# Kernel optimization log

Measured on AMD Instinct MI355X. Metric: run time of the kernel, lower is better.

## Reference

```python
import jax, jax.numpy as jnp
import numpy as np
import math

EMBED_DIM = 1024
NUM_HEADS = 16
HEAD_DIM = EMBED_DIM // NUM_HEADS
B, S = 2, 2048


def setup_inputs() -> dict:
    key = jax.random.key(0)
    ks = jax.random.split(key, 13)
    sc = 1.0 / math.sqrt(EMBED_DIM)
    inp = {
        "query": jax.random.normal(ks[0], (B, S, EMBED_DIM), jnp.float32),
        "key": jax.random.normal(ks[1], (B, S, EMBED_DIM), jnp.float32),
        "value": jax.random.normal(ks[2], (B, S, EMBED_DIM), jnp.float32),
        "input_patch_mask": jax.random.randint(ks[3], (B, S), 0, 2, jnp.int32),
        "Wq": jax.random.normal(ks[4], (EMBED_DIM, EMBED_DIM), jnp.float32) * sc,
        "bq": jnp.zeros((EMBED_DIM,), jnp.float32),
        "Wk": jax.random.normal(ks[5], (EMBED_DIM, EMBED_DIM), jnp.float32) * sc,
        "bk": jnp.zeros((EMBED_DIM,), jnp.float32),
        "Wv": jax.random.normal(ks[6], (EMBED_DIM, EMBED_DIM), jnp.float32) * sc,
        "bv": jnp.zeros((EMBED_DIM,), jnp.float32),
        "Wo": jax.random.normal(ks[7], (EMBED_DIM, EMBED_DIM), jnp.float32) * sc,
        "bo": jnp.zeros((EMBED_DIM,), jnp.float32),
    }
    return inp


def _masked_softmax(scores, mask):
    # Equivalent to masked_fill(-inf) -> softmax -> nan_to_num(0.0):
    # fully-masked rows produce exactly 0, without generating NaNs.
    neg_inf = jnp.array(-jnp.inf, scores.dtype)
    s = jnp.where(mask, scores, neg_inf)
    m = jnp.max(s, axis=-1, keepdims=True)
    m_safe = jnp.where(jnp.isfinite(m), m, jnp.zeros_like(m))
    e = jnp.where(mask, jnp.exp(s - m_safe), 0.0)
    denom = jnp.sum(e, axis=-1, keepdims=True)
    denom = jnp.where(denom == 0.0, 1.0, denom)
    return e / denom


def reference(query, key, value, input_patch_mask, Wq, bq, Wk, bk, Wv, bv, Wo, bo):
    b, s, d = query.shape
    h, hd = NUM_HEADS, HEAD_DIM
    q = (query @ Wq.T + bq).reshape(b, s, h, hd).transpose(0, 2, 1, 3)  # [b,h,s,hd]
    k = (key @ Wk.T + bk).reshape(b, s, h, hd).transpose(0, 2, 1, 3)
    v = (value @ Wv.T + bv).reshape(b, s, h, hd).transpose(0, 2, 1, 3)
    scores = jnp.einsum("bhqd,bhkd->bhqk", q, k) / math.sqrt(hd)
    # mask[b,i,j] = patch_mask[b,i] * patch_mask[b,j]
    mask = (input_patch_mask[:, :, None] * input_patch_mask[:, None, :]) > 0
    attn = _masked_softmax(scores, mask[:, None, :, :])  # dropout in eval mode = identity
    context = jnp.einsum("bhqk,bhkd->bhqd", attn, v)
    context = context.transpose(0, 2, 1, 3).reshape(b, s, d)
    return context @ Wo.T + bo
```

## Files before the change

### kernel.cpp

```cpp
#include <hip/hip_runtime.h>
#include <cstdint>
#include <cstddef>

#define EMBED 1024
#define NHEAD 16
#define HD    64
#define BATCH 2
#define SEQ   2048
#define MROWS (BATCH*SEQ)
#define QSCALE 0.1803368801111137f

typedef __bf16 bf16;
typedef __bf16 bf16x8 __attribute__((ext_vector_type(8)));
typedef float  f32x4  __attribute__((ext_vector_type(4)));
typedef unsigned int u32;

#if __has_builtin(__builtin_amdgcn_exp2f)
#define EXP2(x) __builtin_amdgcn_exp2f(x)
#else
#define EXP2(x) exp2f(x)
#endif

typedef const u32 __attribute__((address_space(1)))* gp_t;
typedef u32 __attribute__((address_space(3)))* lp_t;

__device__ __forceinline__ void g2l16(const void* g, void* l) {
  __builtin_amdgcn_global_load_lds((gp_t)(uintptr_t)g, (lp_t)(u32)(uintptr_t)l, 16, 0, 0);
}

#define MFMA(a, b, c) __builtin_amdgcn_mfma_f32_16x16x32_bf16((a), (b), (c), 0, 0, 0)

#define SZX8 ((MROWS*EMBED)/8)
#define SZW8 ((EMBED*EMBED)/8)

__global__ void cast_all(const float* __restrict__ q, const float* __restrict__ k,
                         const float* __restrict__ v, const float* __restrict__ wq,
                         const float* __restrict__ wk, const float* __restrict__ wv,
                         const float* __restrict__ wo,
                         bf16* xq, bf16* xk, bf16* xv,
                         bf16* wqb, bf16* wkb, bf16* wvb, bf16* wob) {
  int z = blockIdx.y;
  const float* in; bf16* out;
  switch (z) {
    case 0: in = q;  out = xq;  break;
    case 1: in = k;  out = xk;  break;
    case 2: in = v;  out = xv;  break;
    case 3: in = wq; out = wqb; break;
    case 4: in = wk; out = wkb; break;
    case 5: in = wv; out = wvb; break;
    default: in = wo; out = wob; break;
  }
  int n8 = (z < 3) ? SZX8 : SZW8;
  int i = blockIdx.x * blockDim.x + threadIdx.x;
  if (i >= n8) return;
  const float4* p = (const float4*)in;
  float4 a = p[2*i], b = p[2*i+1];
  union { bf16 h[8]; uint4 u; } r;
  r.h[0] = (bf16)a.x; r.h[1] = (bf16)a.y; r.h[2] = (bf16)a.z; r.h[3] = (bf16)a.w;
  r.h[4] = (bf16)b.x; r.h[5] = (bf16)b.y; r.h[6] = (bf16)b.z; r.h[7] = (bf16)b.w;
  ((uint4*)out)[i] = r.u;
}

#define BM 128
#define BN 128
#define BK 32
#define NKI (EMBED/BK)

__device__ __forceinline__ void gemm_core(
    const bf16* __restrict__ A, const bf16* __restrict__ W,
    int m0, int n0, bf16* Al, bf16* Bl, f32x4 (&acc)[4][4])
{
  const int tid  = threadIdx.x;
  const int lane = tid & 63, wid = tid >> 6;
  const int quad = lane >> 4, l16 = lane & 15;
  const int wm = wid >> 1, wn = wid & 1;

  const int R = tid >> 2, Cc = tid & 3;
  const int gcol = (Cc ^ ((R >> 1) & 3)) * 8;
  const bf16* Ag = A + (size_t)(m0 + R) * EMBED + gcol;
  const bf16* Bg = W + (size_t)(n0 + R) * EMBED + gcol;
  bf16* AlW = Al + wid * 512;
  bf16* BlW = Bl + wid * 512;

  g2l16(Ag, AlW);                      g2l16(Ag + (size_t)64*EMBED, AlW + 2048);
  g2l16(Bg, BlW);                      g2l16(Bg + (size_t)64*EMBED, BlW + 2048);
  __syncthreads();

  for (int ki = 0; ki < NKI; ++ki) {
    const int cur = ki & 1;
    if (ki + 1 < NKI) {
      const int nb = cur ^ 1;
      const int k0 = (ki + 1) * BK;
      g2l16(Ag + k0, AlW + nb*4096);
      g2l16(Ag + (size_t)64*EMBED + k0, AlW + nb*4096 + 2048);
      g2l16(Bg + k0, BlW + nb*4096);
      g2l16(Bg + (size_t)64*EMBED + k0, BlW + nb*4096 + 2048);
    }
    const bf16* Ac = Al + cur*4096;
    const bf16* Bc = Bl + cur*4096;
    bf16x8 af[4], bg[4];
#pragma unroll
    for (int i = 0; i < 4; ++i) {
      int ra = wm*64 + i*16 + l16;
      af[i] = *(const bf16x8*)(Ac + ra*32 + ((quad ^ ((ra>>1)&3))*8));
      int rb = wn*64 + i*16 + l16;
      bg[i] = *(const bf16x8*)(Bc + rb*32 + ((quad ^ ((rb>>1)&3))*8));
    }
#pragma unroll
    for (int i = 0; i < 4; ++i)
#pragma unroll
      for (int j = 0; j < 4; ++j)
        acc[i][j] = MFMA(af[i], bg[j], acc[i][j]);
    __syncthreads();
  }
}

__global__ __launch_bounds__(256) void qkv_kernel(
    const bf16* __restrict__ Xq, const bf16* __restrict__ Xk, const bf16* __restrict__ Xv,
    const bf16* __restrict__ Wq, const bf16* __restrict__ Wk, const bf16* __restrict__ Wv,
    const float* __restrict__ bq, const float* __restrict__ bk, const float* __restrict__ bv,
    bf16* __restrict__ Qp, bf16* __restrict__ Kp, bf16* __restrict__ VTg)
{
  __shared__ bf16 Al[2*BM*BK];
  __shared__ bf16 Bl[2*BN*BK];
  const int z = blockIdx.z;
  const bf16* A = z==0 ? Xq : z==1 ? Xk : Wv;
  const bf16* W = z==0 ? Wq : z==1 ? Wk : Xv;
  const float* bias = z==0 ? bq : z==1 ? bk : bv;
  const float scale = (z==0) ? QSCALE : 1.0f;
  const int m0 = (z < 2) ? blockIdx.y * BM : blockIdx.x * BM;
  const int n0 = (z < 2) ? blockIdx.x * BN : blockIdx.y * BN;

  f32x4 acc[4][4] = {};
  gemm_core(A, W, m0, n0, Al, Bl, acc);

  const int lane = threadIdx.x & 63, wid = threadIdx.x >> 6;
  const int quad = lane >> 4, l16 = lane & 15;
  const int wm = wid >> 1, wn = wid & 1;

  if (z < 2) {
#pragma unroll
    for (int i = 0; i < 4; ++i) {
#pragma unroll
      for (int j = 0; j < 4; ++j) {
        int col = n0 + wn*64 + j*16 + l16;
        float bv2 = bias[col];
        bf16* outp = (z == 0) ? Qp : Kp;
#pragma unroll
        for (int r = 0; r < 4; ++r) {
          int row = m0 + wm*64 + i*16 + quad*4 + r;
          outp[(size_t)row*EMBED + col] = (bf16)((acc[i][j][r] + bv2) * scale);
        }
      }
    }
  } else {
    const int tcol0 = n0 + wn*64;
    const int bb   = tcol0 >> 11;
    const int tile = (tcol0 & (SEQ-1)) >> 6;
    const int rA = l16 & 3, qA = l16 >> 2;
    const int pbase = (rA>>1)*32 + qA*8 + (rA&1)*4;
#pragma unroll
    for (int i = 0; i < 4; ++i) {
      float4 bv4 = *(const float4*)&bias[m0 + wm*64 + i*16 + quad*4];
#pragma unroll
      for (int r = 0; r < 4; ++r) {
        int e = m0 + wm*64 + i*16 + quad*4 + r;
        int hh = e >> 6, dd = e & (HD-1);
        float bvr = (r==0) ? bv4.x : (r==1) ? bv4.y : (r==2) ? bv4.z : bv4.w;
        union { bf16 h[4]; uint2 uu; } pk;
#pragma unroll
        for (int j = 0; j < 4; ++j) pk.h[j] = (bf16)(acc[i][j][r] + bvr);
        *(uint2*)&VTg[(((size_t)bb*NHEAD + hh)*HD + dd)*SEQ + tile*64 + pbase] = pk.uu;
      }
    }
  }
}

__global__ __launch_bounds__(256) void oproj_kernel(
    const bf16* __restrict__ Ctx, const bf16* __restrict__ Wo,
    const float* __restrict__ bo, float* __restrict__ out)
{
  __shared__ bf16 Al[2*128*32];
  __shared__ bf16 Bl[2*64*32];
  const int tid  = threadIdx.x;
  const int lane = tid & 63, wid = tid >> 6;
  const int quad = lane >> 4, l16 = lane & 15;
  const int m0 = blockIdx.y * 128, n0 = blockIdx.x * 64;

  const int R = tid >> 2, Cc = tid & 3;
  const int gcol = (Cc ^ ((R >> 1) & 3)) * 8;
  const bf16* Ag = Ctx + (size_t)(m0 + R) * EMBED + gcol;
  const bf16* Bg = Wo  + (size_t)(n0 + R) * EMBED + gcol;
  bf16* AlW = Al + wid * 512;
  bf16* BlW = Bl + wid * 512;

  g2l16(Ag, AlW);  g2l16(Ag + (size_t)64*EMBED, AlW + 2048);
  g2l16(Bg, BlW);
  __syncthreads();

  f32x4 acc[2][4] = {};
  for (int ki = 0; ki < NKI; ++ki) {
    const int cur = ki & 1;
    if (ki + 1 < NKI) {
      const int nb = cur ^ 1;
      const int k0 = (ki + 1) * BK;
      g2l16(Ag + k0, AlW + nb*4096);
      g2l16(Ag + (size_t)64*EMBED + k0, AlW + nb*4096 + 2048);
      g2l16(Bg + k0, BlW + nb*2048);
    }
    const bf16* Ac = Al + cur*4096;
    const bf16* Bc = Bl + cur*2048;
    bf16x8 af[2], bg[4];
#pragma unroll
    for (int u = 0; u < 2; ++u) {
      int ra = wid*32 + u*16 + l16;
      af[u] = *(const bf16x8*)(Ac + ra*32 + ((quad ^ ((ra>>1)&3))*8));
    }
#pragma unroll
    for (int j = 0; j < 4; ++j) {
      int rb = j*16 + l16;
      bg[j] = *(const bf16x8*)(Bc + rb*32 + ((quad ^ ((rb>>1)&3))*8));
    }
#pragma unroll
    for (int u = 0; u < 2; ++u)
#pragma unroll
      for (int j = 0; j < 4; ++j)
        acc[u][j] = MFMA(af[u], bg[j], acc[u][j]);
    __syncthreads();
  }

#pragma unroll
  for (int u = 0; u < 2; ++u)
#pragma unroll
    for (int j = 0; j < 4; ++j) {
      int col = n0 + j*16 + l16;
      float bv = bo[col];
#pragma unroll
      for (int r = 0; r < 4; ++r) {
        int row = m0 + wid*32 + u*16 + quad*4 + r;
        out[(size_t)row*EMBED + col] = (acc[u][j][r] + bv);
      }
    }
}

#define NT  (SEQ/64)

__global__ __launch_bounds__(512, 2) void attn_kernel(
    const bf16* __restrict__ Qp, const bf16* __restrict__ Kp, const bf16* __restrict__ VT,
    const int* __restrict__ pmask, bf16* __restrict__ Ctx)
{
  __shared__ __align__(16) bf16 Kt[2][64*64];
  __shared__ __align__(16) bf16 Vt[3][64*64];

  const int qt = blockIdx.x, h = blockIdx.y, b = blockIdx.z;
  const int tid = threadIdx.x, lane = tid & 63, wid = tid >> 6;
  const int quad = lane >> 4, l16 = lane & 15;
  const int qrow0 = qt*128 + wid*16;

  const size_t qoff = (size_t)(b*SEQ + qrow0 + l16)*EMBED + h*HD;
  bf16x8 qf0 = *(const bf16x8*)(Qp + qoff + quad*8);
  bf16x8 qf1 = *(const bf16x8*)(Qp + qoff + 32 + quad*8);

  int qm[4];
#pragma unroll
  for (int r = 0; r < 4; ++r) qm[r] = pmask[b*SEQ + qrow0 + quad*4 + r];

  bf16 onev = (bf16)1.0f;
  bf16x8 ones = {onev, onev, onev, onev, onev, onev, onev, onev};

  const bf16* Kg  = Kp + (size_t)b*SEQ*EMBED + h*HD;
  const bf16* VTg = VT + (size_t)(b*NHEAD + h)*HD*SEQ;
  const int*  kmb = pmask + b*SEQ;

  const int R = tid >> 3;
  const int Cc = tid & 7;
  const int scol = (Cc ^ (R & 7)) * 8;

  f32x4 o[4] = {};
  f32x4 lacc = {};
  bf16x8 pa0 = {}, pa1 = {};

#define STAGE_K(kt, buf) g2l16(Kg + (size_t)((kt)*64 + R)*EMBED + scol, &Kt[buf][0] + wid*512)
#define STAGE_V(kt, buf) g2l16(VTg + (size_t)R*SEQ + (kt)*64 + scol,    &Vt[buf][0] + wid*512)

  STAGE_K(0, 0);
  STAGE_V(0, 0);
  __syncthreads();

  for (int kt = 0; kt < NT; ++kt) {
    if (kt + 1 < NT) {
      STAGE_K(kt + 1, (kt + 1) & 1);
      STAGE_V(kt + 1, (kt + 1) % 3);
    }

    const bf16* Kc = &Kt[kt & 1][0];
    f32x4 sg[4];
#pragma unroll
    for (int g = 0; g < 4; ++g) {
      int ra = g*16 + l16, sa = ra & 7;
      bf16x8 kfa = *(const bf16x8*)(Kc + ra*64 + ((quad     ^ sa)*8));
      bf16x8 kfb = *(const bf16x8*)(Kc + ra*64 + (((quad+4) ^ sa)*8));
      int4 kq = *(const int4*)(kmb + kt*64 + g*16 + quad*4);
      f32x4 s = {};
      s = MFMA(kfa, qf0, s);
      s = MFMA(kfb, qf1, s);
      sg[g][0] = kq.x ? EXP2(s[0]) : 0.0f;
      sg[g][1] = kq.y ? EXP2(s[1]) : 0.0f;
      sg[g][2] = kq.z ? EXP2(s[2]) : 0.0f;
      sg[g][3] = kq.w ? EXP2(s[3]) : 0.0f;
    }

    if (kt > 0) {
      const bf16* Vc = &Vt[(kt - 1) % 3][0];
      lacc = MFMA(pa0, ones, lacc);
      lacc = MFMA(pa1, ones, lacc);
#pragma unroll
      for (int t = 0; t < 4; ++t) {
        int rd = t*16 + l16, sd = rd & 7;
        bf16x8 vf0 = *(const bf16x8*)(Vc + rd*64 + ((quad     ^ sd)*8));
        bf16x8 vf1 = *(const bf16x8*)(Vc + rd*64 + (((quad+4) ^ sd)*8));
        o[t] = MFMA(pa0, vf0, o[t]);
        o[t] = MFMA(pa1, vf1, o[t]);
      }
    }

    pa0[0] = (bf16)sg[0][0]; pa0[1] = (bf16)sg[1][0]; pa0[2] = (bf16)sg[2][0]; pa0[3] = (bf16)sg[3][0];
    pa0[4] = (bf16)sg[0][1]; pa0[5] = (bf16)sg[1][1]; pa0[6] = (bf16)sg[2][1]; pa0[7] = (bf16)sg[3][1];
    pa1[0] = (bf16)sg[0][2]; pa1[1] = (bf16)sg[1][2]; pa1[2] = (bf16)sg[2][2]; pa1[3] = (bf16)sg[3][2];
    pa1[4] = (bf16)sg[0][3]; pa1[5] = (bf16)sg[1][3]; pa1[6] = (bf16)sg[2][3]; pa1[7] = (bf16)sg[3][3];

    __syncthreads();
  }

  {
    const bf16* Vc = &Vt[(NT - 1) % 3][0];
    lacc = MFMA(pa0, ones, lacc);
    lacc = MFMA(pa1, ones, lacc);
#pragma unroll
    for (int t = 0; t < 4; ++t) {
      int rd = t*16 + l16, sd = rd & 7;
      bf16x8 vf0 = *(const bf16x8*)(Vc + rd*64 + ((quad     ^ sd)*8));
      bf16x8 vf1 = *(const bf16x8*)(Vc + rd*64 + (((quad+4) ^ sd)*8));
      o[t] = MFMA(pa0, vf0, o[t]);
      o[t] = MFMA(pa1, vf1, o[t]);
    }
  }

  float inv[4];
#pragma unroll
  for (int r = 0; r < 4; ++r)
    inv[r] = (qm[r] && lacc[r] > 0.f) ? 1.0f / lacc[r] : 0.0f;

#pragma unroll
  for (int t = 0; t < 4; ++t)
#pragma unroll
    for (int r = 0; r < 4; ++r) {
      int row = b*SEQ + qrow0 + quad*4 + r;
      Ctx[(size_t)row*EMBED + h*HD + t*16 + l16] = (bf16)(o[t][r] * inv[r]);
    }
}

extern "C" void kernel_launch(void* const* d_in, const int* in_sizes, int n_in,
                              void* d_out, int out_size, void* d_ws, size_t ws_size,
                              hipStream_t stream)
{
  const float* query = (const float*)d_in[0];
  const float* key   = (const float*)d_in[1];
  const float* value = (const float*)d_in[2];
  const int*   pm    = (const int*)d_in[3];
  const float* Wq = (const float*)d_in[4];
  const float* bq = (const float*)d_in[5];
  const float* Wk = (const float*)d_in[6];
  const float* bk = (const float*)d_in[7];
  const float* Wv = (const float*)d_in[8];
  const float* bv = (const float*)d_in[9];
  const float* Wo = (const float*)d_in[10];
  const float* bo = (const float*)d_in[11];
  float* out = (float*)d_out;

  const size_t SZ_X = (size_t)MROWS * EMBED;
  const size_t SZ_W = (size_t)EMBED * EMBED;

  bf16* p   = (bf16*)d_ws;
  bf16* Xq  = p; p += SZ_X;
  bf16* Xk  = p; p += SZ_X;
  bf16* Xv  = p; p += SZ_X;
  bf16* Wqb = p; p += SZ_W;
  bf16* Wkb = p; p += SZ_W;
  bf16* Wvb = p; p += SZ_W;
  bf16* Wob = p; p += SZ_W;
  bf16* Qp  = p; p += SZ_X;
  bf16* Kp  = p; p += SZ_X;
  bf16* VTg = p; p += SZ_X;
  bf16* Ctx = p; p += SZ_X;

  dim3 gc((unsigned)(SZX8/256), 7);
  cast_all<<<gc, 256, 0, stream>>>(query, key, value, Wq, Wk, Wv, Wo,
                                   Xq, Xk, Xv, Wqb, Wkb, Wvb, Wob);

  dim3 gq(EMBED/BN, MROWS/BM, 3);
  qkv_kernel<<<gq, 256, 0, stream>>>(Xq, Xk, Xv, Wqb, Wkb, Wvb, bq, bk, bv, Qp, Kp, VTg);

  dim3 ga(SEQ/128, NHEAD, BATCH);
  attn_kernel<<<ga, 512, 0, stream>>>(Qp, Kp, VTg, pm, Ctx);

  dim3 gg(EMBED/64, MROWS/128);
  oproj_kernel<<<gg, 256, 0, stream>>>(Ctx, Wob, bo, out);
}
```

Before: 234.2 us.

## Split attention key tile across wave halves with 32-row query blocks and LDS reduction

```diff
diff --git a/kernel.cpp b/kernel.cpp
--- a/kernel.cpp
+++ b/kernel.cpp
@@ -157,8 +157,7 @@
     const int tcol0 = n0 + wn*64;
     const int bb   = tcol0 >> 11;
     const int tile = (tcol0 & (SEQ-1)) >> 6;
-    const int rA = l16 & 3, qA = l16 >> 2;
-    const int pbase = (rA>>1)*32 + qA*8 + (rA&1)*4;
+    const int pbase = (l16 >> 2)*8 + (l16 & 3)*2;
 #pragma unroll
     for (int i = 0; i < 4; ++i) {
       float4 bv4 = *(const float4*)&bias[m0 + wm*64 + i*16 + quad*4];
@@ -167,10 +166,14 @@
         int e = m0 + wm*64 + i*16 + quad*4 + r;
         int hh = e >> 6, dd = e & (HD-1);
         float bvr = (r==0) ? bv4.x : (r==1) ? bv4.y : (r==2) ? bv4.z : bv4.w;
-        union { bf16 h[4]; uint2 uu; } pk;
-#pragma unroll
-        for (int j = 0; j < 4; ++j) pk.h[j] = (bf16)(acc[i][j][r] + bvr);
-        *(uint2*)&VTg[(((size_t)bb*NHEAD + hh)*HD + dd)*SEQ + tile*64 + pbase] = pk.uu;
+        union { bf16 h[2]; u32 u; } p01, p23;
+        p01.h[0] = (bf16)(acc[i][0][r] + bvr);
+        p01.h[1] = (bf16)(acc[i][1][r] + bvr);
+        p23.h[0] = (bf16)(acc[i][2][r] + bvr);
+        p23.h[1] = (bf16)(acc[i][3][r] + bvr);
+        size_t base = (((size_t)bb*NHEAD + hh)*HD + dd)*SEQ + tile*64;
+        *(u32*)&VTg[base + pbase]      = p01.u;
+        *(u32*)&VTg[base + 32 + pbase] = p23.u;
       }
     }
   }
@@ -249,115 +252,141 @@
     const bf16* __restrict__ Qp, const bf16* __restrict__ Kp, const bf16* __restrict__ VT,
     const int* __restrict__ pmask, bf16* __restrict__ Ctx)
 {
-  __shared__ __align__(16) bf16 Kt[2][64*64];
-  __shared__ __align__(16) bf16 Vt[3][64*64];
+  __shared__ __align__(16) bf16 SM[5*4096];
 
   const int qt = blockIdx.x, h = blockIdx.y, b = blockIdx.z;
   const int tid = threadIdx.x, lane = tid & 63, wid = tid >> 6;
   const int quad = lane >> 4, l16 = lane & 15;
-  const int qrow0 = qt*128 + wid*16;
-
-  const size_t qoff = (size_t)(b*SEQ + qrow0 + l16)*EMBED + h*HD;
-  bf16x8 qf0 = *(const bf16x8*)(Qp + qoff + quad*8);
-  bf16x8 qf1 = *(const bf16x8*)(Qp + qoff + 32 + quad*8);
-
-  int qm[4];
-#pragma unroll
-  for (int r = 0; r < 4; ++r) qm[r] = pmask[b*SEQ + qrow0 + quad*4 + r];
+  const int w4 = wid & 3, h2 = wid >> 2;
+  const int qrow0 = qt*128 + w4*32;
+
+  bf16x8 qf[2][2];
+#pragma unroll
+  for (int qg = 0; qg < 2; ++qg) {
+    const size_t qoff = (size_t)(b*SEQ + qrow0 + qg*16 + l16)*EMBED + h*HD;
+    qf[qg][0] = *(const bf16x8*)(Qp + qoff + quad*8);
+    qf[qg][1] = *(const bf16x8*)(Qp + qoff + 32 + quad*8);
+  }
 
   bf16 onev = (bf16)1.0f;
   bf16x8 ones = {onev, onev, onev, onev, onev, onev, onev, onev};
 
   const bf16* Kg  = Kp + (size_t)b*SEQ*EMBED + h*HD;
   const bf16* VTg = VT + (size_t)(b*NHEAD + h)*HD*SEQ;
-  const int*  kmb = pmask + b*SEQ;
+  const int*  kmw = pmask + b*SEQ + h2*32 + quad*4;
 
   const int R = tid >> 3;
   const int Cc = tid & 7;
   const int scol = (Cc ^ (R & 7)) * 8;
 
-  f32x4 o[4] = {};
-  f32x4 lacc = {};
-  bf16x8 pa0 = {}, pa1 = {};
-
-#define STAGE_K(kt, buf) g2l16(Kg + (size_t)((kt)*64 + R)*EMBED + scol, &Kt[buf][0] + wid*512)
-#define STAGE_V(kt, buf) g2l16(VTg + (size_t)R*SEQ + (kt)*64 + scol,    &Vt[buf][0] + wid*512)
+  f32x4 o[2][4] = {};
+  f32x4 lacc[2] = {};
+  bf16x8 pa[2] = {};
+
+#define STAGE_K(kt, buf) g2l16(Kg + (size_t)((kt)*64 + R)*EMBED + scol, SM + (buf)*4096 + wid*512)
+#define STAGE_V(kt, buf) g2l16(VTg + (size_t)R*SEQ + (kt)*64 + scol,    SM + 8192 + (buf)*4096 + wid*512)
+
+  int4 kq0 = *(const int4*)(kmw);
+  int4 kq1 = *(const int4*)(kmw + 16);
 
   STAGE_K(0, 0);
   STAGE_V(0, 0);
   __syncthreads();
 
   for (int kt = 0; kt < NT; ++kt) {
+    const int ktn = (kt + 1 < NT) ? kt + 1 : 0;
+    int4 kqn0 = *(const int4*)(kmw + ktn*64);
+    int4 kqn1 = *(const int4*)(kmw + ktn*64 + 16);
     if (kt + 1 < NT) {
       STAGE_K(kt + 1, (kt + 1) & 1);
       STAGE_V(kt + 1, (kt + 1) % 3);
     }
 
-    const bf16* Kc = &Kt[kt & 1][0];
-    f32x4 sg[4];
-#pragma unroll
-    for (int g = 0; g < 4; ++g) {
-      int ra = g*16 + l16, sa = ra & 7;
-      bf16x8 kfa = *(const bf16x8*)(Kc + ra*64 + ((quad     ^ sa)*8));
-      bf16x8 kfb = *(const bf16x8*)(Kc + ra*64 + (((quad+4) ^ sa)*8));
-      int4 kq = *(const int4*)(kmb + kt*64 + g*16 + quad*4);
-      f32x4 s = {};
-      s = MFMA(kfa, qf0, s);
-      s = MFMA(kfb, qf1, s);
-      sg[g][0] = kq.x ? EXP2(s[0]) : 0.0f;
-      sg[g][1] = kq.y ? EXP2(s[1]) : 0.0f;
-      sg[g][2] = kq.z ? EXP2(s[2]) : 0.0f;
-      sg[g][3] = kq.w ? EXP2(s[3]) : 0.0f;
-    }
-
     if (kt > 0) {
-      const bf16* Vc = &Vt[(kt - 1) % 3][0];
-      lacc = MFMA(pa0, ones, lacc);
-      lacc = MFMA(pa1, ones, lacc);
+      const bf16* Vc = SM + 8192 + ((kt - 1) % 3)*4096;
+      lacc[0] = MFMA(pa[0], ones, lacc[0]);
+      lacc[1] = MFMA(pa[1], ones, lacc[1]);
 #pragma unroll
       for (int t = 0; t < 4; ++t) {
         int rd = t*16 + l16, sd = rd & 7;
-        bf16x8 vf0 = *(const bf16x8*)(Vc + rd*64 + ((quad     ^ sd)*8));
-        bf16x8 vf1 = *(const bf16x8*)(Vc + rd*64 + (((quad+4) ^ sd)*8));
-        o[t] = MFMA(pa0, vf0, o[t]);
-        o[t] = MFMA(pa1, vf1, o[t]);
+        bf16x8 vf = *(const bf16x8*)(Vc + rd*64 + (((h2*4 + quad) ^ sd)*8));
+        o[0][t] = MFMA(pa[0], vf, o[0][t]);
+        o[1][t] = MFMA(pa[1], vf, o[1][t]);
       }
     }
 
-    pa0[0] = (bf16)sg[0][0]; pa0[1] = (bf16)sg[1][0]; pa0[2] = (bf16)sg[2][0]; pa0[3] = (bf16)sg[3][0];
-    pa0[4] = (bf16)sg[0][1]; pa0[5] = (bf16)sg[1][1]; pa0[6] = (bf16)sg[2][1]; pa0[7] = (bf16)sg[3][1];
-    pa1[0] = (bf16)sg[0][2]; pa1[1] = (bf16)sg[1][2]; pa1[2] = (bf16)sg[2][2]; pa1[3] = (bf16)sg[3][2];
-    pa1[4] = (bf16)sg[0][3]; pa1[5] = (bf16)sg[1][3]; pa1[6] = (bf16)sg[2][3]; pa1[7] = (bf16)sg[3][3];
-
+    const bf16* Kc = SM + (kt & 1)*4096;
+#pragma unroll
+    for (int kg = 0; kg < 2; ++kg) {
+      int ra = h2*32 + kg*16 + l16, sa = ra & 7;
+      bf16x8 kfa = *(const bf16x8*)(Kc + ra*64 + ((quad       ^ sa)*8));
+      bf16x8 kfb = *(const bf16x8*)(Kc + ra*64 + (((quad + 4) ^ sa)*8));
+      int4 kq = kg ? kq1 : kq0;
+#pragma unroll
+      for (int qg = 0; qg < 2; ++qg) {
+        f32x4 s = {};
+        s = MFMA(kfa, qf[qg][0], s);
+        s = MFMA(kfb, qf[qg][1], s);
+        pa[qg][0 + kg] = (bf16)(kq.x ? EXP2(s[0]) : 0.0f);
+        pa[qg][2 + kg] = (bf16)(kq.y ? EXP2(s[1]) : 0.0f);
+        pa[qg][4 + kg] = (bf16)(kq.z ? EXP2(s[2]) : 0.0f);
+        pa[qg][6 + kg] = (bf16)(kq.w ? EXP2(s[3]) : 0.0f);
+      }
+    }
+
+    kq0 = kqn0; kq1 = kqn1;
     __syncthreads();
   }
 
   {
-    const bf16* Vc = &Vt[(NT - 1) % 3][0];
-    lacc = MFMA(pa0, ones, lacc);
-    lacc = MFMA(pa1, ones, lacc);
+    const bf16* Vc = SM + 8192 + ((NT - 1) % 3)*4096;
+    lacc[0] = MFMA(pa[0], ones, lacc[0]);
+    lacc[1] = MFMA(pa[1], ones, lacc[1]);
 #pragma unroll
     for (int t = 0; t < 4; ++t) {
       int rd = t*16 + l16, sd = rd & 7;
-      bf16x8 vf0 = *(const bf16x8*)(Vc + rd*64 + ((quad     ^ sd)*8));
-      bf16x8 vf1 = *(const bf16x8*)(Vc + rd*64 + (((quad+4) ^ sd)*8));
-      o[t] = MFMA(pa0, vf0, o[t]);
-      o[t] = MFMA(pa1, vf1, o[t]);
-    }
-  }
-
-  float inv[4];
-#pragma unroll
-  for (int r = 0; r < 4; ++r)
-    inv[r] = (qm[r] && lacc[r] > 0.f) ? 1.0f / lacc[r] : 0.0f;
-
-#pragma unroll
-  for (int t = 0; t < 4; ++t)
-#pragma unroll
-    for (int r = 0; r < 4; ++r) {
-      int row = b*SEQ + qrow0 + quad*4 + r;
-      Ctx[(size_t)row*EMBED + h*HD + t*16 + l16] = (bf16)(o[t][r] * inv[r]);
-    }
+      bf16x8 vf = *(const bf16x8*)(Vc + rd*64 + (((h2*4 + quad) ^ sd)*8));
+      o[0][t] = MFMA(pa[0], vf, o[0][t]);
+      o[1][t] = MFMA(pa[1], vf, o[1][t]);
+    }
+  }
+
+  __syncthreads();
+  f32x4* rp = (f32x4*)SM;
+  const int idx = w4*64 + lane;
+  if (h2 == 1) {
+#pragma unroll
+    for (int qg = 0; qg < 2; ++qg) {
+#pragma unroll
+      for (int t = 0; t < 4; ++t) rp[(qg*4 + t)*256 + idx] = o[qg][t];
+      rp[2048 + qg*256 + idx] = lacc[qg];
+    }
+  }
+  __syncthreads();
+  if (h2 == 0) {
+#pragma unroll
+    for (int qg = 0; qg < 2; ++qg) {
+      lacc[qg] += rp[2048 + qg*256 + idx];
+#pragma unroll
+      for (int t = 0; t < 4; ++t) o[qg][t] += rp[(qg*4 + t)*256 + idx];
+    }
+#pragma unroll
+    for (int qg = 0; qg < 2; ++qg) {
+      int4 qm = *(const int4*)(pmask + b*SEQ + qrow0 + qg*16 + quad*4);
+      float inv[4];
+      inv[0] = (qm.x && lacc[qg][0] > 0.f) ? 1.0f / lacc[qg][0] : 0.0f;
+      inv[1] = (qm.y && lacc[qg][1] > 0.f) ? 1.0f / lacc[qg][1] : 0.0f;
+      inv[2] = (qm.z && lacc[qg][2] > 0.f) ? 1.0f / lacc[qg][2] : 0.0f;
+      inv[3] = (qm.w && lacc[qg][3] > 0.f) ? 1.0f / lacc[qg][3] : 0.0f;
+#pragma unroll
+      for (int t = 0; t < 4; ++t)
+#pragma unroll
+        for (int r = 0; r < 4; ++r) {
+          int row = b*SEQ + qrow0 + qg*16 + quad*4 + r;
+          Ctx[(size_t)row*EMBED + h*HD + t*16 + l16] = (bf16)(o[qg][t][r] * inv[r]);
+        }
+    }
+  }
 }
 
 extern "C" void kernel_launch(void* const* d_in, const int* in_sizes, int n_in,
```

Result: no change. 233.1 us (-0.5%).
